# Kernel optimization log

Measured on AMD Instinct MI355X. Metric: run time of the kernel, lower is better.

Reference implementation:

```python
import jax, jax.numpy as jnp
import numpy as np

B, S, D, H = 2, 2048, 1024, 16
DK = D // H
NEG = -1e9


def setup_inputs() -> dict:
    key = jax.random.key(0)
    ks = jax.random.split(key, 12)
    scale = 1.0 / np.sqrt(D)
    inp = {
        'Q': jax.random.normal(ks[0], (B, S, D), jnp.float32),
        'K': jax.random.normal(ks[1], (B, S, D), jnp.float32),
        'V': jax.random.normal(ks[2], (B, S, D), jnp.float32),
        'mask': jnp.tril(jnp.ones((S, S), jnp.int32))[None, None],  # (1,1,S,S) causal
        # torch nn.Linear layout: W has shape (out, in), y = x @ W.T + b
        'WQ': jax.random.normal(ks[3], (D, D), jnp.float32) * scale,
        'bQ': jnp.zeros((D,), jnp.float32),
        'WK': jax.random.normal(ks[4], (D, D), jnp.float32) * scale,
        'bK': jnp.zeros((D,), jnp.float32),
        'WV': jax.random.normal(ks[5], (D, D), jnp.float32) * scale,
        'bV': jnp.zeros((D,), jnp.float32),
        'WO': jax.random.normal(ks[6], (D, D), jnp.float32) * scale,
        'bO': jnp.zeros((D,), jnp.float32),
    }
    return inp


def reference(Q, K, V, mask, WQ, bQ, WK, bK, WV, bV, WO, bO):
    # projections (torch Linear: x @ W.T + b), then split heads -> (B,H,S,DK)
    def split_heads(x):
        return x.reshape(B, S, H, DK).transpose(0, 2, 1, 3)

    Qh = split_heads(Q @ WQ.T + bQ)
    Kh = split_heads(K @ WK.T + bK)
    Vh = split_heads(V @ WV.T + bV)

    scores = jnp.einsum('bhqd,bhkd->bhqk', Qh, Kh) / jnp.sqrt(jnp.float32(DK))
    scores = jnp.where(mask == 0, NEG, scores)
    attn = jax.nn.softmax(scores, axis=-1)  # (B,H,S,S)
    ctx = jnp.einsum('bhqk,bhkd->bhqd', attn, Vh)
    concat = ctx.transpose(0, 2, 1, 3).reshape(B, S, D)
    out = concat @ WO.T + bO
    return out, attn
```

## Files before the change

kernel.cpp:

```cpp
#include <hip/hip_runtime.h>
#include <hip/hip_bf16.h>
#include <cstdint>
#include <cstddef>

#define S_ 2048
#define D_ 1024
#define H_ 16
#define DK_ 64
#define B_ 2

typedef unsigned short u16;
typedef __attribute__((ext_vector_type(8))) short bf16x8;
typedef __attribute__((ext_vector_type(4))) float f32x4;

__device__ inline u16 f2bf(float f) {
    union { float f; unsigned u; } c; c.f = f;
    unsigned u = c.u;
    unsigned r = (u + 0x7fffu + ((u >> 16) & 1u)) >> 16;
    return (u16)r;
}

__device__ inline uint4 cvt8(const float* __restrict__ src) {
    float4 f0 = *(const float4*)(src);
    float4 f1 = *(const float4*)(src + 4);
    union { u16 h[8]; uint4 v; } u;
    u.h[0] = f2bf(f0.x); u.h[1] = f2bf(f0.y); u.h[2] = f2bf(f0.z); u.h[3] = f2bf(f0.w);
    u.h[4] = f2bf(f1.x); u.h[5] = f2bf(f1.y); u.h[6] = f2bf(f1.z); u.h[7] = f2bf(f1.w);
    return u.v;
}

__device__ inline unsigned pkbf(float a, float b) {
    unsigned r;
    asm("v_cvt_pk_bf16_f32 %0, %1, %2" : "=v"(r) : "v"(a), "v"(b));
    return r;
}

typedef __attribute__((address_space(3))) void lds_void;
typedef __attribute__((address_space(1))) const void glob_void;
__device__ __forceinline__ void glds16(const u16* g, u16* l) {
#if __has_builtin(__builtin_amdgcn_global_load_lds)
    __builtin_amdgcn_global_load_lds((glob_void*)g, (lds_void*)l, 16, 0, 0);
#else
    ((uint4*)l)[threadIdx.x & 63] = *(const uint4*)g;
#endif
}

__device__ __forceinline__ bf16x8 rd64(const u16* arr, int row, int k) {
    return *(const bf16x8*)((const char*)arr + (row << 7)
             + ((k << 1) ^ ((row & 7) << 4)));
}
__device__ __forceinline__ bf16x8 rd128(const u16* arr, int row, int k) {
    return *(const bf16x8*)((const char*)arr + (row << 8)
             + ((k << 1) ^ ((row & 7) << 4)));
}

__global__ void __launch_bounds__(256)
cvt_all(const float* __restrict__ Q, const float* __restrict__ K,
        const float* __restrict__ V,
        const float* __restrict__ WQ, const float* __restrict__ WK,
        const float* __restrict__ WV, const float* __restrict__ WO,
        u16* __restrict__ Qb, u16* __restrict__ Kb, u16* __restrict__ Vb,
        u16* __restrict__ Wb)
{
    const size_t QN = 524288;
    const size_t WN = 131072;
    size_t u = (size_t)blockIdx.x * 256 + threadIdx.x;
    const size_t total = 3 * QN + 4 * WN;
    const size_t stride = (size_t)gridDim.x * 256;
    for (; u < total; u += stride) {
        const float* s; u16* d; size_t off;
        if (u < 3 * QN) {
            size_t seg = u / QN;
            off = (u - seg * QN) << 3;
            s = (seg == 0) ? Q : (seg == 1) ? K : V;
            d = (seg == 0) ? Qb : (seg == 1) ? Kb : Vb;
        } else {
            size_t w = u - 3 * QN;
            size_t seg = w / WN;
            off = (w - seg * WN) << 3;
            s = (seg == 0) ? WQ : (seg == 1) ? WK : (seg == 2) ? WV : WO;
            d = Wb + seg * 1048576;
        }
        *(uint4*)&d[off] = cvt8(s + off);
    }
}

__device__ __forceinline__ void gemm_stage(
    const u16* __restrict__ A, const u16* __restrict__ Bm,
    int m0, int n0, int k0, int tid, u16* As, u16* Bs)
{
#pragma unroll
    for (int it = 0; it < 4; ++it) {
        int linear = it * 256 + tid;
        int row = linear >> 3, c = linear & 7;
        glds16(&A[(size_t)(m0 + row) * 1024 + k0 + ((c ^ (row & 7)) << 3)],
               &As[(size_t)(it * 256 + (tid & ~63)) << 3]);
        glds16(&Bm[(size_t)(n0 + row) * 1024 + k0 + ((c ^ (row & 7)) << 3)],
               &Bs[(size_t)(it * 256 + (tid & ~63)) << 3]);
    }
}

__device__ __forceinline__ void gemm_core(
    const u16* __restrict__ A, const u16* __restrict__ Bm,
    int m0, int n0, int tid, u16* As, u16* Bs, f32x4 (&acc)[4][4])
{
    const int lane = tid & 63;
    const int wave = tid >> 6;
    const int wm = wave >> 1, wn = wave & 1;
    const int fr = lane & 15, fq = lane >> 4;

    gemm_stage(A, Bm, m0, n0, 0, tid, As, Bs);
    __syncthreads();

    for (int t = 0; t < 16; ++t) {
        const int cur = t & 1;
        u16* Ac = As + cur * 8192;
        u16* Bc = Bs + cur * 8192;
        if (t + 1 < 16)
            gemm_stage(A, Bm, m0, n0, (t + 1) * 64, tid,
                       As + (cur ^ 1) * 8192, Bs + (cur ^ 1) * 8192);
#pragma unroll
        for (int ks = 0; ks < 64; ks += 32) {
            bf16x8 af[4], bfv[4];
#pragma unroll
            for (int mt = 0; mt < 4; ++mt)
                af[mt] = rd64(Ac, wm * 64 + mt * 16 + fr, ks + (fq << 3));
#pragma unroll
            for (int nt = 0; nt < 4; ++nt)
                bfv[nt] = rd64(Bc, wn * 64 + nt * 16 + fr, ks + (fq << 3));
#pragma unroll
            for (int mt = 0; mt < 4; ++mt)
#pragma unroll
                for (int nt = 0; nt < 4; ++nt)
                    acc[mt][nt] = __builtin_amdgcn_mfma_f32_16x16x32_bf16(
                        bfv[nt], af[mt], acc[mt][nt], 0, 0, 0);
        }
        __syncthreads();
    }
}

__global__ void __launch_bounds__(256)
proj_qkv(const u16* __restrict__ Qb, const u16* __restrict__ Kb,
         const u16* __restrict__ Vb, const u16* __restrict__ Wb,
         const float* __restrict__ bQ, const float* __restrict__ bK,
         const float* __restrict__ bV,
         u16* __restrict__ Qh, u16* __restrict__ Kh, u16* __restrict__ Vt)
{
    __shared__ __align__(16) u16 As[2 * 128 * 64];
    __shared__ __align__(16) u16 Bs[2 * 128 * 64];

    const int tid  = threadIdx.x;
    const int lane = tid & 63;
    const int wave = tid >> 6;
    const int wm = wave >> 1, wn = wave & 1;
    const int fr = lane & 15, fq = lane >> 4;
    const int m0 = blockIdx.y * 128;
    const int n0 = blockIdx.x * 128;
    const int z  = blockIdx.z;

    const u16* A = (z == 0) ? Qb : (z == 1) ? Kb : Vb;
    const u16* W = Wb + (size_t)z * 1048576;
    const float* bias = (z == 0) ? bQ : (z == 1) ? bK : bV;
    u16* O = (z == 0) ? Qh : (z == 1) ? Kh : Vt;

    f32x4 acc[4][4];
#pragma unroll
    for (int i = 0; i < 4; ++i)
#pragma unroll
        for (int j = 0; j < 4; ++j) acc[i][j] = (f32x4){0.f, 0.f, 0.f, 0.f};

    gemm_core(A, W, m0, n0, tid, As, Bs, acc);

#pragma unroll
    for (int mt = 0; mt < 4; ++mt) {
#pragma unroll
        for (int nt = 0; nt < 4; ++nt) {
            int row  = m0 + wm * 64 + mt * 16 + fr;
            int colb = n0 + wn * 64 + nt * 16 + (fq << 2);
            float4 b4 = *(const float4*)&bias[colb];
            u16 h[4];
            h[0] = f2bf(acc[mt][nt][0] + b4.x);
            h[1] = f2bf(acc[mt][nt][1] + b4.y);
            h[2] = f2bf(acc[mt][nt][2] + b4.z);
            h[3] = f2bf(acc[mt][nt][3] + b4.w);
            if (z < 2) {
                size_t addr = ((size_t)(row >> 11) << 21) + ((size_t)(colb >> 6) << 17)
                            + ((size_t)(row & 2047) << 6) + (size_t)(colb & 63);
                uint2 p; p.x = (unsigned)h[0] | ((unsigned)h[1] << 16);
                         p.y = (unsigned)h[2] | ((unsigned)h[3] << 16);
                *(uint2*)&O[addr] = p;
            } else {
#pragma unroll
                for (int r = 0; r < 4; ++r) {
                    int col = colb + r;
                    size_t addr = ((size_t)(row >> 11) << 21) + ((size_t)(col >> 6) << 17)
                                + ((size_t)(col & 63) << 11) + (size_t)(row & 2047);
                    O[addr] = h[r];
                }
            }
        }
    }
}

__global__ void __launch_bounds__(256)
out_gemm(const u16* __restrict__ Cc, const u16* __restrict__ WOb,
         const float* __restrict__ bO, float* __restrict__ C)
{
    __shared__ __align__(16) u16 As[2 * 128 * 64];
    __shared__ __align__(16) u16 Bs[2 * 128 * 64];

    const int tid  = threadIdx.x;
    const int lane = tid & 63;
    const int wave = tid >> 6;
    const int wm = wave >> 1, wn = wave & 1;
    const int fr = lane & 15, fq = lane >> 4;
    const int m0 = blockIdx.y * 128;
    const int n0 = blockIdx.x * 128;

    f32x4 acc[4][4];
#pragma unroll
    for (int i = 0; i < 4; ++i)
#pragma unroll
        for (int j = 0; j < 4; ++j) acc[i][j] = (f32x4){0.f, 0.f, 0.f, 0.f};

    gemm_core(Cc, WOb, m0, n0, tid, As, Bs, acc);

#pragma unroll
    for (int mt = 0; mt < 4; ++mt) {
#pragma unroll
        for (int nt = 0; nt < 4; ++nt) {
            int row  = m0 + wm * 64 + mt * 16 + fr;
            int colb = n0 + wn * 64 + nt * 16 + (fq << 2);
            float4 b4 = *(const float4*)&bO[colb];
            float4 v;
            v.x = acc[mt][nt][0] + b4.x;
            v.y = acc[mt][nt][1] + b4.y;
            v.z = acc[mt][nt][2] + b4.z;
            v.w = acc[mt][nt][3] + b4.w;
            *(float4*)&C[(size_t)row * D_ + colb] = v;
        }
    }
}

__global__ void __launch_bounds__(256, 2)
attn_all(const u16* __restrict__ Qh, const u16* __restrict__ Kh,
         const u16* __restrict__ Vt,
         float* __restrict__ attn, u16* __restrict__ Cc)
{
    __shared__ __align__(16) u16 Qs[128 * 64];
    __shared__ __align__(16) u16 Ks[128 * 64];
    __shared__ __align__(16) u16 Vs[64 * 128];
    __shared__ __align__(16) u16 Ps[128 * 128];
    float* rowsum = (float*)Vs;

    const int tid  = threadIdx.x;
    const int lane = tid & 63;
    const int wave = tid >> 6;
    const int wm = wave >> 1, wn = wave & 1;
    const int bx = blockIdx.x;
    const int bh = blockIdx.y;
    const int qt = (bh & 16) ? (15 - bx) : bx;
    const int fr = lane & 15, fq = lane >> 4;

    const u16* Qbase = Qh + (size_t)bh * S_ * DK_ + (size_t)qt * 128 * DK_;
    const u16* Kbase = Kh + (size_t)bh * S_ * DK_;
    const u16* Vbase = Vt + (size_t)bh * (size_t)DK_ * S_;
    float* out = attn + (size_t)bh * S_ * S_;

#pragma unroll
    for (int it = 0; it < 4; ++it) {
        int linear = it * 256 + tid;
        int row = linear >> 3, c = linear & 7;
        glds16(&Qbase[(size_t)row * 64 + ((c ^ (row & 7)) << 3)],
               &Qs[(size_t)(it * 256 + (tid & ~63)) << 3]);
        glds16(&Kbase[(size_t)row * 64 + ((c ^ (row & 7)) << 3)],
               &Ks[(size_t)(it * 256 + (tid & ~63)) << 3]);
    }
    if (tid < 128) rowsum[tid] = 0.f;
    __syncthreads();

    float rs[4] = {0.f, 0.f, 0.f, 0.f};

    for (int kt = 0; kt <= qt; ++kt) {
        f32x4 acc[4][4];
#pragma unroll
        for (int i = 0; i < 4; ++i)
#pragma unroll
            for (int j = 0; j < 4; ++j) acc[i][j] = (f32x4){0.f, 0.f, 0.f, 0.f};

#pragma unroll
        for (int ks = 0; ks < 64; ks += 32) {
            bf16x8 kf4[4], qf4[4];
#pragma unroll
            for (int i = 0; i < 4; ++i)
                kf4[i] = rd64(Ks, wm * 64 + i * 16 + fr, ks + (fq << 3));
#pragma unroll
            for (int j = 0; j < 4; ++j)
                qf4[j] = rd64(Qs, wn * 64 + j * 16 + fr, ks + (fq << 3));
#pragma unroll
            for (int i = 0; i < 4; ++i)
#pragma unroll
                for (int j = 0; j < 4; ++j)
                    acc[i][j] = __builtin_amdgcn_mfma_f32_16x16x32_bf16(
                        kf4[i], qf4[j], acc[i][j], 0, 0, 0);
        }
        __syncthreads();
        if (kt < qt) {
#pragma unroll
            for (int it = 0; it < 4; ++it) {
                int linear = it * 256 + tid;
                int row = linear >> 3, c = linear & 7;
                glds16(&Kbase[(size_t)(kt + 1) * 128 * 64 + (size_t)row * 64
                              + ((c ^ (row & 7)) << 3)],
                       &Ks[(size_t)(it * 256 + (tid & ~63)) << 3]);
            }
        }

        const bool diag = (kt == qt);
#pragma unroll
        for (int kf = 0; kf < 4; ++kf) {
#pragma unroll
            for (int qf = 0; qf < 4; ++qf) {
                const int kb = wm * 64 + kf * 16, qb = wn * 64 + qf * 16;
                if (!diag || kb < qb) {
#pragma unroll
                    for (int r = 0; r < 4; ++r)
                        rs[qf] += __expf(acc[kf][qf][r] * 0.125f);
                } else if (diag && kb == qb) {
#pragma unroll
                    for (int r = 0; r < 4; ++r)
                        if ((fq << 2) + r <= fr)
                            rs[qf] += __expf(acc[kf][qf][r] * 0.125f);
                }
            }
        }
        __syncthreads();
    }

#pragma unroll
    for (int qf = 0; qf < 4; ++qf) {
        float v = rs[qf];
        v += __shfl_xor(v, 16, 64);
        v += __shfl_xor(v, 32, 64);
        if (lane < 16) atomicAdd(&rowsum[wn * 64 + qf * 16 + lane], v);
    }
    __syncthreads();

    float rcp_l[4];
#pragma unroll
    for (int qf = 0; qf < 4; ++qf)
        rcp_l[qf] = 1.0f / rowsum[wn * 64 + qf * 16 + fr];
    __syncthreads();

    f32x4 cacc[4][2];
#pragma unroll
    for (int i = 0; i < 4; ++i)
#pragma unroll
        for (int j = 0; j < 2; ++j) cacc[i][j] = (f32x4){0.f, 0.f, 0.f, 0.f};

#pragma unroll
    for (int it = 0; it < 4; ++it) {
        int linear = it * 256 + tid;
        int row = linear >> 3, c = linear & 7;
        glds16(&Kbase[(size_t)row * 64 + ((c ^ (row & 7)) << 3)],
               &Ks[(size_t)(it * 256 + (tid & ~63)) << 3]);
        int rv = linear >> 4, cv = linear & 15;
        glds16(&Vbase[(size_t)rv * S_ + ((cv ^ (rv & 7)) << 3)],
               &Vs[(size_t)(it * 256 + (tid & ~63)) << 3]);
    }
    __syncthreads();

    for (int kt = 0; kt <= qt; ++kt) {
        f32x4 acc[4][4];
#pragma unroll
        for (int i = 0; i < 4; ++i)
#pragma unroll
            for (int j = 0; j < 4; ++j) acc[i][j] = (f32x4){0.f, 0.f, 0.f, 0.f};

#pragma unroll
        for (int ks = 0; ks < 64; ks += 32) {
            bf16x8 kf4[4], qf4[4];
#pragma unroll
            for (int i = 0; i < 4; ++i)
                kf4[i] = rd64(Ks, wm * 64 + i * 16 + fr, ks + (fq << 3));
#pragma unroll
            for (int j = 0; j < 4; ++j)
                qf4[j] = rd64(Qs, wn * 64 + j * 16 + fr, ks + (fq << 3));
#pragma unroll
            for (int i = 0; i < 4; ++i)
#pragma unroll
                for (int j = 0; j < 4; ++j)
                    acc[i][j] = __builtin_amdgcn_mfma_f32_16x16x32_bf16(
                        kf4[i], qf4[j], acc[i][j], 0, 0, 0);
        }
        __syncthreads();
        if (kt < qt) {
#pragma unroll
            for (int it = 0; it < 4; ++it) {
                int linear = it * 256 + tid;
                int row = linear >> 3, c = linear & 7;
                glds16(&Kbase[(size_t)(kt + 1) * 128 * 64 + (size_t)row * 64
                              + ((c ^ (row & 7)) << 3)],
                       &Ks[(size_t)(it * 256 + (tid & ~63)) << 3]);
            }
        }

        const bool diag = (kt == qt);
#pragma unroll
        for (int kf = 0; kf < 4; ++kf) {
#pragma unroll
            for (int qf = 0; qf < 4; ++qf) {
                const int kb = wm * 64 + kf * 16, qb = wn * 64 + qf * 16;
                const int qrow = qb + fr;
                float4 p4;
                if (!diag || kb < qb) {
                    p4.x = __expf(acc[kf][qf][0] * 0.125f) * rcp_l[qf];
                    p4.y = __expf(acc[kf][qf][1] * 0.125f) * rcp_l[qf];
                    p4.z = __expf(acc[kf][qf][2] * 0.125f) * rcp_l[qf];
                    p4.w = __expf(acc[kf][qf][3] * 0.125f) * rcp_l[qf];
                } else if (kb > qb) {
                    p4 = (float4){0.f, 0.f, 0.f, 0.f};
                } else {
#pragma unroll
                    for (int r = 0; r < 4; ++r) {
                        float e = __expf(acc[kf][qf][r] * 0.125f) * rcp_l[qf];
                        ((float*)&p4)[r] = ((fq << 2) + r <= fr) ? e : 0.f;
                    }
                }
                *(float4*)&out[(size_t)(qt * 128 + qrow) * S_ + kt * 128 + kb + (fq << 2)] = p4;
                uint2 pk;
                pk.x = pkbf(p4.x, p4.y);
                pk.y = pkbf(p4.z, p4.w);
                *(uint2*)((char*)Ps + (qrow << 8)
                          + (((kb + (fq << 2)) << 1) ^ ((qrow & 7) << 4))) = pk;
            }
        }
        __syncthreads();

#pragma unroll
        for (int ks4 = 0; ks4 < 4; ++ks4) {
            bf16x8 pf[4], vf[2];
            const int kk = ks4 * 32 + (fq << 3);
#pragma unroll
            for (int mt = 0; mt < 4; ++mt)
                pf[mt] = rd128(Ps, wm * 64 + mt * 16 + fr, kk);
#pragma unroll
            for (int nt = 0; nt < 2; ++nt)
                vf[nt] = rd128(Vs, wn * 32 + nt * 16 + fr, kk);
#pragma unroll
            for (int mt = 0; mt < 4; ++mt)
#pragma unroll
                for (int nt = 0; nt < 2; ++nt)
                    cacc[mt][nt] = __builtin_amdgcn_mfma_f32_16x16x32_bf16(
                        pf[mt], vf[nt], cacc[mt][nt], 0, 0, 0);
        }
        __syncthreads();
        if (kt < qt) {
#pragma unroll
            for (int it = 0; it < 4; ++it) {
                int linear = it * 256 + tid;
                int rv = linear >> 4, cv = linear & 15;
                glds16(&Vbase[(size_t)rv * S_ + (kt + 1) * 128 + ((cv ^ (rv & 7)) << 3)],
                       &Vs[(size_t)(it * 256 + (tid & ~63)) << 3]);
            }
        }
    }

#pragma unroll
    for (int mt = 0; mt < 4; ++mt)
#pragma unroll
        for (int nt = 0; nt < 2; ++nt)
#pragma unroll
            for (int r = 0; r < 4; ++r) {
                int row = wm * 64 + mt * 16 + (fq << 2) + r;
                int col = wn * 32 + nt * 16 + fr;
                size_t addr = (size_t)(bh >> 4) * S_ * D_ + (size_t)(bh & 15) * DK_
                            + (size_t)(qt * 128 + row) * D_ + col;
                Cc[addr] = f2bf(cacc[mt][nt][r]);
            }

    float4 z4 = {0.f, 0.f, 0.f, 0.f};
    for (int kt2 = qt + 1; kt2 < S_ / 128; ++kt2) {
#pragma unroll
        for (int i = 0; i < 16; ++i) {
            int linear = i * 256 + tid;
            int row = linear >> 5;
            int c   = (linear & 31) << 2;
            *(float4*)&out[(size_t)(qt * 128 + row) * S_ + kt2 * 128 + c] = z4;
        }
    }
}

extern "C" void kernel_launch(void* const* d_in, const int* in_sizes, int n_in,
                              void* d_out, int out_size, void* d_ws, size_t ws_size,
                              hipStream_t stream)
{
    const float* Q  = (const float*)d_in[0];
    const float* K  = (const float*)d_in[1];
    const float* V  = (const float*)d_in[2];
    const float* WQ = (const float*)d_in[4];
    const float* bQ = (const float*)d_in[5];
    const float* WK = (const float*)d_in[6];
    const float* bK = (const float*)d_in[7];
    const float* WV = (const float*)d_in[8];
    const float* bV = (const float*)d_in[9];
    const float* WO = (const float*)d_in[10];
    const float* bO = (const float*)d_in[11];

    float* outF  = (float*)d_out;
    float* attnF = outF + (size_t)B_ * S_ * D_;

    const size_t SZ = (size_t)B_ * S_ * D_;
    u16* Qh = (u16*)d_ws;
    u16* Kh = Qh + SZ;
    u16* Vt = Kh + SZ;
    u16* Cc = Vt + SZ;
    u16* Qb = Cc + SZ;
    u16* Kb = Qb + SZ;
    u16* Vb = Kb + SZ;
    u16* Wb = Vb + SZ;

    dim3 blk(256, 1, 1);

    cvt_all<<<dim3(1024, 1, 1), blk, 0, stream>>>(
        Q, K, V, WQ, WK, WV, WO, Qb, Kb, Vb, Wb);

    proj_qkv<<<dim3(8, 32, 3), blk, 0, stream>>>(
        Qb, Kb, Vb, Wb, bQ, bK, bV, Qh, Kh, Vt);

    attn_all<<<dim3(S_ / 128, B_ * H_, 1), blk, 0, stream>>>(
        Qh, Kh, Vt, attnF, Cc);

    out_gemm<<<dim3(8, 32, 1), blk, 0, stream>>>(
        Cc, Wb + 3 * 1048576, bO, outF);
}
```

Baseline: 774.0 us.

## Split softmax row-sum pass into a separate triangular-tile kernel with atomics

The first pass of the attention kernel, which computes QK^T and the exp row sums, moves into a new kernel launched over all 136 causal (q,k) tile pairs per head. Each block adds its partial sums into a global buffer with atomics, and that buffer is zeroed inside the conversion kernel. This spreads the row-sum work across many blocks instead of serialising it per query tile and load-imbalancing by qt, and attn_all now only does the normalized pass. The GEMM core also drops LDS double buffering for a single buffer, and s_setprio hints are added around the MFMA sections. The cost is QK^T recomputed in a separate launch, extra atomics, and less load/compute overlap in the projection GEMMs.

```diff
diff --git a/kernel.cpp b/kernel.cpp
--- a/kernel.cpp
+++ b/kernel.cpp
@@ -60,43 +60,31 @@
         const float* __restrict__ WQ, const float* __restrict__ WK,
         const float* __restrict__ WV, const float* __restrict__ WO,
         u16* __restrict__ Qb, u16* __restrict__ Kb, u16* __restrict__ Vb,
-        u16* __restrict__ Wb)
+        u16* __restrict__ Wb, float* __restrict__ sums)
 {
     const size_t QN = 524288;
     const size_t WN = 131072;
+    const size_t ZN = 16384;
     size_t u = (size_t)blockIdx.x * 256 + threadIdx.x;
-    const size_t total = 3 * QN + 4 * WN;
+    const size_t total = 3 * QN + 4 * WN + ZN;
     const size_t stride = (size_t)gridDim.x * 256;
     for (; u < total; u += stride) {
-        const float* s; u16* d; size_t off;
         if (u < 3 * QN) {
             size_t seg = u / QN;
-            off = (u - seg * QN) << 3;
-            s = (seg == 0) ? Q : (seg == 1) ? K : V;
-            d = (seg == 0) ? Qb : (seg == 1) ? Kb : Vb;
-        } else {
+            size_t off = (u - seg * QN) << 3;
+            const float* s = (seg == 0) ? Q : (seg == 1) ? K : V;
+            u16* d = (seg == 0) ? Qb : (seg == 1) ? Kb : Vb;
+            *(uint4*)&d[off] = cvt8(s + off);
+        } else if (u < 3 * QN + 4 * WN) {
             size_t w = u - 3 * QN;
             size_t seg = w / WN;
-            off = (w - seg * WN) << 3;
-            s = (seg == 0) ? WQ : (seg == 1) ? WK : (seg == 2) ? WV : WO;
-            d = Wb + seg * 1048576;
-        }
-        *(uint4*)&d[off] = cvt8(s + off);
-    }
-}
-
-__device__ __forceinline__ void gemm_stage(
-    const u16* __restrict__ A, const u16* __restrict__ Bm,
-    int m0, int n0, int k0, int tid, u16* As, u16* Bs)
-{
-#pragma unroll
-    for (int it = 0; it < 4; ++it) {
-        int linear = it * 256 + tid;
-        int row = linear >> 3, c = linear & 7;
-        glds16(&A[(size_t)(m0 + row) * 1024 + k0 + ((c ^ (row & 7)) << 3)],
-               &As[(size_t)(it * 256 + (tid & ~63)) << 3]);
-        glds16(&Bm[(size_t)(n0 + row) * 1024 + k0 + ((c ^ (row & 7)) << 3)],
-               &Bs[(size_t)(it * 256 + (tid & ~63)) << 3]);
+            size_t off = (w - seg * WN) << 3;
+            const float* s = (seg == 0) ? WQ : (seg == 1) ? WK : (seg == 2) ? WV : WO;
+            *(uint4*)&(Wb + seg * 1048576)[off] = cvt8(s + off);
+        } else {
+            uint4 z = {0u, 0u, 0u, 0u};
+            ((uint4*)sums)[u - 3 * QN - 4 * WN] = z;
+        }
     }
 }
 
@@ -109,25 +97,28 @@
     const int wm = wave >> 1, wn = wave & 1;
     const int fr = lane & 15, fq = lane >> 4;
 
-    gemm_stage(A, Bm, m0, n0, 0, tid, As, Bs);
-    __syncthreads();
-
-    for (int t = 0; t < 16; ++t) {
-        const int cur = t & 1;
-        u16* Ac = As + cur * 8192;
-        u16* Bc = Bs + cur * 8192;
-        if (t + 1 < 16)
-            gemm_stage(A, Bm, m0, n0, (t + 1) * 64, tid,
-                       As + (cur ^ 1) * 8192, Bs + (cur ^ 1) * 8192);
+    for (int k0 = 0; k0 < 1024; k0 += 64) {
+        __syncthreads();
+#pragma unroll
+        for (int it = 0; it < 4; ++it) {
+            int linear = it * 256 + tid;
+            int row = linear >> 3, c = linear & 7;
+            glds16(&A[(size_t)(m0 + row) * 1024 + k0 + ((c ^ (row & 7)) << 3)],
+                   &As[(size_t)(it * 256 + (tid & ~63)) << 3]);
+            glds16(&Bm[(size_t)(n0 + row) * 1024 + k0 + ((c ^ (row & 7)) << 3)],
+                   &Bs[(size_t)(it * 256 + (tid & ~63)) << 3]);
+        }
+        __syncthreads();
+        __builtin_amdgcn_s_setprio(1);
 #pragma unroll
         for (int ks = 0; ks < 64; ks += 32) {
             bf16x8 af[4], bfv[4];
 #pragma unroll
             for (int mt = 0; mt < 4; ++mt)
-                af[mt] = rd64(Ac, wm * 64 + mt * 16 + fr, ks + (fq << 3));
+                af[mt] = rd64(As, wm * 64 + mt * 16 + fr, ks + (fq << 3));
 #pragma unroll
             for (int nt = 0; nt < 4; ++nt)
-                bfv[nt] = rd64(Bc, wn * 64 + nt * 16 + fr, ks + (fq << 3));
+                bfv[nt] = rd64(Bs, wn * 64 + nt * 16 + fr, ks + (fq << 3));
 #pragma unroll
             for (int mt = 0; mt < 4; ++mt)
 #pragma unroll
@@ -135,7 +126,7 @@
                     acc[mt][nt] = __builtin_amdgcn_mfma_f32_16x16x32_bf16(
                         bfv[nt], af[mt], acc[mt][nt], 0, 0, 0);
         }
-        __syncthreads();
+        __builtin_amdgcn_s_setprio(0);
     }
 }
 
@@ -146,8 +137,8 @@
          const float* __restrict__ bV,
          u16* __restrict__ Qh, u16* __restrict__ Kh, u16* __restrict__ Vt)
 {
-    __shared__ __align__(16) u16 As[2 * 128 * 64];
-    __shared__ __align__(16) u16 Bs[2 * 128 * 64];
+    __shared__ __align__(16) u16 As[128 * 64];
+    __shared__ __align__(16) u16 Bs[128 * 64];
 
     const int tid  = threadIdx.x;
     const int lane = tid & 63;
@@ -206,8 +197,8 @@
 out_gemm(const u16* __restrict__ Cc, const u16* __restrict__ WOb,
          const float* __restrict__ bO, float* __restrict__ C)
 {
-    __shared__ __align__(16) u16 As[2 * 128 * 64];
-    __shared__ __align__(16) u16 Bs[2 * 128 * 64];
+    __shared__ __align__(16) u16 As[128 * 64];
+    __shared__ __align__(16) u16 Bs[128 * 64];
 
     const int tid  = threadIdx.x;
     const int lane = tid & 63;
@@ -242,16 +233,103 @@
     }
 }
 
+__global__ void __launch_bounds__(256)
+attn_sums(const u16* __restrict__ Qh, const u16* __restrict__ Kh,
+          float* __restrict__ sums)
+{
+    __shared__ __align__(16) u16 Qs[128 * 64];
+    __shared__ __align__(16) u16 Ks[128 * 64];
+
+    const int tid  = threadIdx.x;
+    const int lane = tid & 63;
+    const int wave = tid >> 6;
+    const int wm = wave >> 1, wn = wave & 1;
+    const int fr = lane & 15, fq = lane >> 4;
+    const int p  = blockIdx.x;
+    const int bh = blockIdx.y;
+
+    int qt = 0;
+    while ((qt + 1) * (qt + 2) / 2 <= p) ++qt;
+    const int kt = p - qt * (qt + 1) / 2;
+
+    const u16* Qbase = Qh + (size_t)bh * S_ * DK_ + (size_t)qt * 128 * DK_;
+    const u16* Kbase = Kh + (size_t)bh * S_ * DK_ + (size_t)kt * 128 * DK_;
+
+#pragma unroll
+    for (int it = 0; it < 4; ++it) {
+        int linear = it * 256 + tid;
+        int row = linear >> 3, c = linear & 7;
+        glds16(&Qbase[(size_t)row * 64 + ((c ^ (row & 7)) << 3)],
+               &Qs[(size_t)(it * 256 + (tid & ~63)) << 3]);
+        glds16(&Kbase[(size_t)row * 64 + ((c ^ (row & 7)) << 3)],
+               &Ks[(size_t)(it * 256 + (tid & ~63)) << 3]);
+    }
+    __syncthreads();
+
+    f32x4 acc[4][4];
+#pragma unroll
+    for (int i = 0; i < 4; ++i)
+#pragma unroll
+        for (int j = 0; j < 4; ++j) acc[i][j] = (f32x4){0.f, 0.f, 0.f, 0.f};
+
+    __builtin_amdgcn_s_setprio(1);
+#pragma unroll
+    for (int ks = 0; ks < 64; ks += 32) {
+        bf16x8 kf4[4], qf4[4];
+#pragma unroll
+        for (int i = 0; i < 4; ++i)
+            kf4[i] = rd64(Ks, wm * 64 + i * 16 + fr, ks + (fq << 3));
+#pragma unroll
+        for (int j = 0; j < 4; ++j)
+            qf4[j] = rd64(Qs, wn * 64 + j * 16 + fr, ks + (fq << 3));
+#pragma unroll
+        for (int i = 0; i < 4; ++i)
+#pragma unroll
+            for (int j = 0; j < 4; ++j)
+                acc[i][j] = __builtin_amdgcn_mfma_f32_16x16x32_bf16(
+                    kf4[i], qf4[j], acc[i][j], 0, 0, 0);
+    }
+    __builtin_amdgcn_s_setprio(0);
+
+    const bool diag = (kt == qt);
+    float rs[4] = {0.f, 0.f, 0.f, 0.f};
+#pragma unroll
+    for (int kf = 0; kf < 4; ++kf) {
+#pragma unroll
+        for (int qf = 0; qf < 4; ++qf) {
+            const int kb = wm * 64 + kf * 16, qb = wn * 64 + qf * 16;
+            if (!diag || kb < qb) {
+#pragma unroll
+                for (int r = 0; r < 4; ++r)
+                    rs[qf] += __expf(acc[kf][qf][r] * 0.125f);
+            } else if (diag && kb == qb) {
+#pragma unroll
+                for (int r = 0; r < 4; ++r)
+                    if ((fq << 2) + r <= fr)
+                        rs[qf] += __expf(acc[kf][qf][r] * 0.125f);
+            }
+        }
+    }
+
+#pragma unroll
+    for (int qf = 0; qf < 4; ++qf) {
+        float v = rs[qf];
+        v += __shfl_xor(v, 16, 64);
+        v += __shfl_xor(v, 32, 64);
+        if (lane < 16)
+            atomicAdd(&sums[(size_t)bh * S_ + qt * 128 + wn * 64 + qf * 16 + lane], v);
+    }
+}
+
 __global__ void __launch_bounds__(256, 2)
 attn_all(const u16* __restrict__ Qh, const u16* __restrict__ Kh,
-         const u16* __restrict__ Vt,
+         const u16* __restrict__ Vt, const float* __restrict__ sums,
          float* __restrict__ attn, u16* __restrict__ Cc)
 {
     __shared__ __align__(16) u16 Qs[128 * 64];
     __shared__ __align__(16) u16 Ks[128 * 64];
     __shared__ __align__(16) u16 Vs[64 * 128];
     __shared__ __align__(16) u16 Ps[128 * 128];
-    float* rowsum = (float*)Vs;
 
     const int tid  = threadIdx.x;
     const int lane = tid & 63;
@@ -275,11 +353,23 @@
                &Qs[(size_t)(it * 256 + (tid & ~63)) << 3]);
         glds16(&Kbase[(size_t)row * 64 + ((c ^ (row & 7)) << 3)],
                &Ks[(size_t)(it * 256 + (tid & ~63)) << 3]);
-    }
-    if (tid < 128) rowsum[tid] = 0.f;
+        int rv = linear >> 4, cv = linear & 15;
+        glds16(&Vbase[(size_t)rv * S_ + ((cv ^ (rv & 7)) << 3)],
+               &Vs[(size_t)(it * 256 + (tid & ~63)) << 3]);
+    }
+
+    float rcp_l[4];
+#pragma unroll
+    for (int qf = 0; qf < 4; ++qf)
+        rcp_l[qf] = 1.0f / sums[(size_t)bh * S_ + qt * 128 + wn * 64 + qf * 16 + fr];
+
+    f32x4 cacc[4][2];
+#pragma unroll
+    for (int i = 0; i < 4; ++i)
+#pragma unroll
+        for (int j = 0; j < 2; ++j) cacc[i][j] = (f32x4){0.f, 0.f, 0.f, 0.f};
+
     __syncthreads();
-
-    float rs[4] = {0.f, 0.f, 0.f, 0.f};
 
     for (int kt = 0; kt <= qt; ++kt) {
         f32x4 acc[4][4];
@@ -288,6 +378,7 @@
 #pragma unroll
             for (int j = 0; j < 4; ++j) acc[i][j] = (f32x4){0.f, 0.f, 0.f, 0.f};
 
+        __builtin_amdgcn_s_setprio(1);
 #pragma unroll
         for (int ks = 0; ks < 64; ks += 32) {
             bf16x8 kf4[4], qf4[4];
@@ -304,95 +395,7 @@
                     acc[i][j] = __builtin_amdgcn_mfma_f32_16x16x32_bf16(
                         kf4[i], qf4[j], acc[i][j], 0, 0, 0);
         }
-        __syncthreads();
-        if (kt < qt) {
-#pragma unroll
-            for (int it = 0; it < 4; ++it) {
-                int linear = it * 256 + tid;
-                int row = linear >> 3, c = linear & 7;
-                glds16(&Kbase[(size_t)(kt + 1) * 128 * 64 + (size_t)row * 64
-                              + ((c ^ (row & 7)) << 3)],
-                       &Ks[(size_t)(it * 256 + (tid & ~63)) << 3]);
-            }
-        }
-
-        const bool diag = (kt == qt);
-#pragma unroll
-        for (int kf = 0; kf < 4; ++kf) {
-#pragma unroll
-            for (int qf = 0; qf < 4; ++qf) {
-                const int kb = wm * 64 + kf * 16, qb = wn * 64 + qf * 16;
-                if (!diag || kb < qb) {
-#pragma unroll
-                    for (int r = 0; r < 4; ++r)
-                        rs[qf] += __expf(acc[kf][qf][r] * 0.125f);
-                } else if (diag && kb == qb) {
-#pragma unroll
-                    for (int r = 0; r < 4; ++r)
-                        if ((fq << 2) + r <= fr)
-                            rs[qf] += __expf(acc[kf][qf][r] * 0.125f);
-                }
-            }
-        }
-        __syncthreads();
-    }
-
-#pragma unroll
-    for (int qf = 0; qf < 4; ++qf) {
-        float v = rs[qf];
-        v += __shfl_xor(v, 16, 64);
-        v += __shfl_xor(v, 32, 64);
-        if (lane < 16) atomicAdd(&rowsum[wn * 64 + qf * 16 + lane], v);
-    }
-    __syncthreads();
-
-    float rcp_l[4];
-#pragma unroll
-    for (int qf = 0; qf < 4; ++qf)
-        rcp_l[qf] = 1.0f / rowsum[wn * 64 + qf * 16 + fr];
-    __syncthreads();
-
-    f32x4 cacc[4][2];
-#pragma unroll
-    for (int i = 0; i < 4; ++i)
-#pragma unroll
-        for (int j = 0; j < 2; ++j) cacc[i][j] = (f32x4){0.f, 0.f, 0.f, 0.f};
-
-#pragma unroll
-    for (int it = 0; it < 4; ++it) {
-        int linear = it * 256 + tid;
-        int row = linear >> 3, c = linear & 7;
-        glds16(&Kbase[(size_t)row * 64 + ((c ^ (row & 7)) << 3)],
-               &Ks[(size_t)(it * 256 + (tid & ~63)) << 3]);
-        int rv = linear >> 4, cv = linear & 15;
-        glds16(&Vbase[(size_t)rv * S_ + ((cv ^ (rv & 7)) << 3)],
-               &Vs[(size_t)(it * 256 + (tid & ~63)) << 3]);
-    }
-    __syncthreads();
-
-    for (int kt = 0; kt <= qt; ++kt) {
-        f32x4 acc[4][4];
-#pragma unroll
-        for (int i = 0; i < 4; ++i)
-#pragma unroll
-            for (int j = 0; j < 4; ++j) acc[i][j] = (f32x4){0.f, 0.f, 0.f, 0.f};
-
-#pragma unroll
-        for (int ks = 0; ks < 64; ks += 32) {
-            bf16x8 kf4[4], qf4[4];
-#pragma unroll
-            for (int i = 0; i < 4; ++i)
-                kf4[i] = rd64(Ks, wm * 64 + i * 16 + fr, ks + (fq << 3));
-#pragma unroll
-            for (int j = 0; j < 4; ++j)
-                qf4[j] = rd64(Qs, wn * 64 + j * 16 + fr, ks + (fq << 3));
-#pragma unroll
-            for (int i = 0; i < 4; ++i)
-#pragma unroll
-                for (int j = 0; j < 4; ++j)
-                    acc[i][j] = __builtin_amdgcn_mfma_f32_16x16x32_bf16(
-                        kf4[i], qf4[j], acc[i][j], 0, 0, 0);
-        }
+        __builtin_amdgcn_s_setprio(0);
         __syncthreads();
         if (kt < qt) {
 #pragma unroll
@@ -437,6 +440,7 @@
         }
         __syncthreads();
 
+        __builtin_amdgcn_s_setprio(1);
 #pragma unroll
         for (int ks4 = 0; ks4 < 4; ++ks4) {
             bf16x8 pf[4], vf[2];
@@ -454,6 +458,7 @@
                     cacc[mt][nt] = __builtin_amdgcn_mfma_f32_16x16x32_bf16(
                         pf[mt], vf[nt], cacc[mt][nt], 0, 0, 0);
         }
+        __builtin_amdgcn_s_setprio(0);
         __syncthreads();
         if (kt < qt) {
 #pragma unroll
@@ -519,17 +524,20 @@
     u16* Kb = Qb + SZ;
     u16* Vb = Kb + SZ;
     u16* Wb = Vb + SZ;
+    float* sums = (float*)(Wb + 4 * 1048576);
 
     dim3 blk(256, 1, 1);
 
     cvt_all<<<dim3(1024, 1, 1), blk, 0, stream>>>(
-        Q, K, V, WQ, WK, WV, WO, Qb, Kb, Vb, Wb);
+        Q, K, V, WQ, WK, WV, WO, Qb, Kb, Vb, Wb, sums);
 
     proj_qkv<<<dim3(8, 32, 3), blk, 0, stream>>>(
         Qb, Kb, Vb, Wb, bQ, bK, bV, Qh, Kh, Vt);
 
+    attn_sums<<<dim3(136, 32, 1), blk, 0, stream>>>(Qh, Kh, sums);
+
     attn_all<<<dim3(S_ / 128, B_ * H_, 1), blk, 0, stream>>>(
-        Qh, Kh, Vt, attnF, Cc);
+        Qh, Kh, Vt, sums, attnF, Cc);
 
     out_gemm<<<dim3(8, 32, 1), blk, 0, stream>>>(
         Cc, Wb + 3 * 1048576, bO, outF);
```

New measurement: 770.8 us. Within noise of the previous version (-0.4%).
